# Kernel optimization log

Hardware: AMD Instinct MI355X
Metric: run time of the kernel (lower is better)

Reference implementation:

```python
import jax, jax.numpy as jnp
import numpy as np

NEG_INF_SCALE = -1e9  # matches mask * -1000000000.0 in the original


def setup_inputs() -> dict:
    key = jax.random.key(0)
    k1, k2, k3, k4 = jax.random.split(key, 4)
    B, H, S, D = 2, 16, 2048, 64
    return {
        "query": jax.random.normal(k1, (B, H, S, D), dtype=jnp.float32),
        "key": jax.random.normal(k2, (B, H, S, D), dtype=jnp.float32),
        "value": jax.random.normal(k3, (B, H, S, D), dtype=jnp.float32),
        "mask": jax.random.randint(k4, (B, 1, 1, S), 0, 2, dtype=jnp.int32),
    }


def reference(query, key, value, mask):
    head_dimension = query.shape[-1]
    scale = 1.0 / jnp.sqrt(jnp.float32(head_dimension))
    # (b h q d),(b h k d) -> (b h q k)
    logits = jnp.einsum("bhqd,bhkd->bhqk", query, key) * scale
    logits = logits + mask.astype(logits.dtype) * NEG_INF_SCALE
    attention_weights = jax.nn.softmax(logits, axis=-1)
    # (b h q k),(b h k d) -> (b h q d)
    output = jnp.einsum("bhqk,bhkd->bhqd", attention_weights, value)
    return output, attention_weights
```

## Files before the change

### kernel.cpp

```cpp
#include <hip/hip_runtime.h>

#define SEQ   2048
#define DIM   64
#define NB    2
#define NH    16
#define NHEAD (NB * NH)
#define BQ    128
#define BK    64
#define NKT   (SEQ / BK)
#define NQT   (SEQ / BQ)
#define QSCALE 0.18033688011112042f

typedef float  f32x4  __attribute__((ext_vector_type(4)));
typedef short  bf16x8 __attribute__((ext_vector_type(8)));
typedef unsigned short u16;
typedef u16    u16x4  __attribute__((ext_vector_type(4)));
typedef u16    u16x8  __attribute__((ext_vector_type(8)));
typedef unsigned int u32x4 __attribute__((ext_vector_type(4)));

__device__ __forceinline__ short f2bf(float x) {
    unsigned u = __float_as_uint(x);
    return (short)((u + 0x7FFFu + ((u >> 16) & 1u)) >> 16);
}

__device__ __forceinline__ unsigned cvtpk(float lo, float hi) {
    unsigned r;
    asm("v_cvt_pk_bf16_f32 %0, %1, %2" : "=v"(r) : "v"(lo), "v"(hi));
    return r;
}

__device__ __forceinline__ void gll16(const void* g, void* l) {
    __builtin_amdgcn_global_load_lds(
        (const __attribute__((address_space(1))) unsigned int*)g,
        (__attribute__((address_space(3))) unsigned int*)l, 16, 0, 0);
}

__global__ __launch_bounds__(256)
void conv_k_kernel(const float* __restrict__ K, u16* __restrict__ Kp)
{
    const int idx  = (int)blockIdx.x * 256 + (int)threadIdx.x;
    const int lane = idx & 63;
    const int s    = (idx >> 6) & 7;
    const int kt   = (idx >> 9) & 31;
    const int h    = idx >> 14;
    const int mrow = lane & 15;
    const int kg4  = (lane >> 4) << 2;
    const int row  = (s >> 1) * 16 + mrow;
    const int cb   = (s & 1) * 32 + kg4;

    const float* src = K + ((size_t)h * SEQ + (size_t)kt * 64 + row) * DIM + cb;
    const float4 a = *reinterpret_cast<const float4*>(src);
    const float4 b = *reinterpret_cast<const float4*>(src + 16);
    u16x8 o;
    o[0] = (u16)f2bf(a.x); o[1] = (u16)f2bf(a.y); o[2] = (u16)f2bf(a.z); o[3] = (u16)f2bf(a.w);
    o[4] = (u16)f2bf(b.x); o[5] = (u16)f2bf(b.y); o[6] = (u16)f2bf(b.z); o[7] = (u16)f2bf(b.w);
    *reinterpret_cast<u16x8*>(Kp + (size_t)idx * 8) = o;
}

__global__ __launch_bounds__(256)
void conv_v_kernel(const float* __restrict__ V, u16* __restrict__ Vp)
{
    const int idx  = (int)blockIdx.x * 256 + (int)threadIdx.x;
    const int lane = idx & 63;
    const int s    = (idx >> 6) & 7;
    const int kt   = (idx >> 9) & 31;
    const int h    = idx >> 14;
    const int mrow = lane & 15;
    const int kg4  = (lane >> 4) << 2;
    const int rd   = (s >> 1) * 16 + mrow;
    const int cb   = (s & 1) * 32 + kg4;

    const float* vb = V + ((size_t)h * SEQ + (size_t)kt * 64) * DIM;
    u16x8 o;
    #pragma unroll
    for (int j = 0; j < 4; ++j) {
        o[j]     = (u16)f2bf(vb[(size_t)(cb + j) * DIM + rd]);
        o[4 + j] = (u16)f2bf(vb[(size_t)(cb + 16 + j) * DIM + rd]);
    }
    *reinterpret_cast<u16x8*>(Vp + (size_t)idx * 8) = o;
}

__global__ __launch_bounds__(512, 4)
void sdpa_main_kernel(const float* __restrict__ Qp, const u16* __restrict__ Kp,
                      const u16* __restrict__ Vp, const int* __restrict__ Mp,
                      float* __restrict__ Op, float* __restrict__ Pg_)
{
    __shared__ u16   Ks[3][4096];
    __shared__ u16   Vs[3][4096];
    __shared__ float Fb[SEQ];
    __shared__ u16   Pst[8][16][68];

    const int tid  = (int)threadIdx.x;
    const int lane = tid & 63;
    const int w    = tid >> 6;
    const int mrow = lane & 15;
    const int kg4  = (lane >> 4) << 2;

    const int bid  = (int)blockIdx.x;
    const int xcd  = bid & 7;
    const int slot = bid >> 3;
    const int bh   = xcd * 4 + (slot >> 4);
    const int qt   = slot & 15;

    const size_t headoff = (size_t)bh * SEQ * DIM;
    const float* Qg = Qp + headoff + (size_t)qt * BQ * DIM;
    const u16*   Kh = Kp + (size_t)bh * NKT * 4096;
    const u16*   Vh = Vp + (size_t)bh * NKT * 4096;
    const int*   Mg = Mp + (size_t)(bh / NH) * SEQ;
    float*       Og = Op + headoff + (size_t)qt * BQ * DIM;
    float*       Pg = Pg_ + ((size_t)bh * SEQ + (size_t)qt * BQ) * SEQ;

    {
        const int4 m0 = *reinterpret_cast<const int4*>(Mg + tid * 4);
        float4 f0;
        f0.x = m0.x ? -1.0e9f : 0.0f; f0.y = m0.y ? -1.0e9f : 0.0f;
        f0.z = m0.z ? -1.0e9f : 0.0f; f0.w = m0.w ? -1.0e9f : 0.0f;
        *reinterpret_cast<float4*>(&Fb[tid * 4]) = f0;
    }

    bf16x8 qf0, qf1;
    {
        const float* qrow = Qg + (size_t)(w * 16 + mrow) * DIM;
        const float4 a = *reinterpret_cast<const float4*>(qrow + kg4);
        const float4 b = *reinterpret_cast<const float4*>(qrow + 16 + kg4);
        const float4 c = *reinterpret_cast<const float4*>(qrow + 32 + kg4);
        const float4 d = *reinterpret_cast<const float4*>(qrow + 48 + kg4);
        qf0[0] = f2bf(a.x * QSCALE); qf0[1] = f2bf(a.y * QSCALE);
        qf0[2] = f2bf(a.z * QSCALE); qf0[3] = f2bf(a.w * QSCALE);
        qf0[4] = f2bf(b.x * QSCALE); qf0[5] = f2bf(b.y * QSCALE);
        qf0[6] = f2bf(b.z * QSCALE); qf0[7] = f2bf(b.w * QSCALE);
        qf1[0] = f2bf(c.x * QSCALE); qf1[1] = f2bf(c.y * QSCALE);
        qf1[2] = f2bf(c.z * QSCALE); qf1[3] = f2bf(c.w * QSCALE);
        qf1[4] = f2bf(d.x * QSCALE); qf1[5] = f2bf(d.y * QSCALE);
        qf1[6] = f2bf(d.z * QSCALE); qf1[7] = f2bf(d.w * QSCALE);
    }
    __syncthreads();

    const int so  = tid * 8;
    const int lo8 = lane * 8;

    gll16(Kh + so, &Ks[0][so]);
    gll16(Kh + 4096 + so, &Ks[1][so]);

    float lsum = 0.f;
    int bcur = 0, bpre = 2;

    for (int kt = 0; kt < NKT; ++kt) {
        asm volatile("s_waitcnt vmcnt(1)" ::: "memory");
        __builtin_amdgcn_s_barrier();
        gll16(Kh + (size_t)((kt + 2) & (NKT - 1)) * 4096 + so, &Ks[bpre][so]);
        __builtin_amdgcn_sched_barrier(0);

        const u16* kp = &Ks[bcur][lo8];
        const int k0 = kt * BK;
        #pragma unroll
        for (int t = 0; t < 4; ++t) {
            const bf16x8 kf0 = *reinterpret_cast<const bf16x8*>(kp + (2 * t) * 512);
            const bf16x8 kf1 = *reinterpret_cast<const bf16x8*>(kp + (2 * t + 1) * 512);
            f32x4 a = {0.f, 0.f, 0.f, 0.f};
            a = __builtin_amdgcn_mfma_f32_16x16x32_bf16(kf0, qf0, a, 0, 0, 0);
            a = __builtin_amdgcn_mfma_f32_16x16x32_bf16(kf1, qf1, a, 0, 0, 0);
            const float4 b = *reinterpret_cast<const float4*>(&Fb[k0 + t * 16 + kg4]);
            lsum += __builtin_amdgcn_exp2f(a[0] + b.x);
            lsum += __builtin_amdgcn_exp2f(a[1] + b.y);
            lsum += __builtin_amdgcn_exp2f(a[2] + b.z);
            lsum += __builtin_amdgcn_exp2f(a[3] + b.w);
        }

        bcur = (bcur == 2) ? 0 : bcur + 1;
        bpre = (bpre == 2) ? 0 : bpre + 1;
    }

    asm volatile("s_waitcnt vmcnt(0)" ::: "memory");

    lsum += __shfl_xor(lsum, 16);
    lsum += __shfl_xor(lsum, 32);
    const float rinv = 1.0f / lsum;

    __builtin_amdgcn_s_barrier();

    f32x4 oacc[4];
    #pragma unroll
    for (int n = 0; n < 4; ++n) {
        oacc[n][0] = 0.f; oacc[n][1] = 0.f; oacc[n][2] = 0.f; oacc[n][3] = 0.f;
    }

    gll16(Kh + so, &Ks[0][so]);
    gll16(Vh + so, &Vs[0][so]);
    gll16(Kh + 4096 + so, &Ks[1][so]);
    gll16(Vh + 4096 + so, &Vs[1][so]);
    asm volatile("s_waitcnt vmcnt(2)" ::: "memory");
    __builtin_amdgcn_s_barrier();
    bcur = 0; bpre = 2;

    float* PgW = Pg + (size_t)(w * 16) * SEQ;

    for (int kt = 0; kt < NKT; ++kt) {
        if (kt == 1) { asm volatile("s_waitcnt vmcnt(6)" ::: "memory"); }
        else         { asm volatile("s_waitcnt vmcnt(10)" ::: "memory"); }
        __builtin_amdgcn_s_barrier();
        {
            const size_t nt = (size_t)((kt + 2) & (NKT - 1)) * 4096;
            gll16(Kh + nt + so, &Ks[bpre][so]);
            gll16(Vh + nt + so, &Vs[bpre][so]);
        }
        __builtin_amdgcn_sched_barrier(0);

        const u16* kp = &Ks[bcur][lo8];
        const u16* vp = &Vs[bcur][lo8];
        const int k0 = kt * BK;
        bf16x8 pf0, pf1;

        #pragma unroll
        for (int half = 0; half < 2; ++half) {
            f32x4 p[2];
            #pragma unroll
            for (int i = 0; i < 2; ++i) {
                const int t = half * 2 + i;
                const bf16x8 kf0 = *reinterpret_cast<const bf16x8*>(kp + (2 * t) * 512);
                const bf16x8 kf1 = *reinterpret_cast<const bf16x8*>(kp + (2 * t + 1) * 512);
                f32x4 a = {0.f, 0.f, 0.f, 0.f};
                a = __builtin_amdgcn_mfma_f32_16x16x32_bf16(kf0, qf0, a, 0, 0, 0);
                a = __builtin_amdgcn_mfma_f32_16x16x32_bf16(kf1, qf1, a, 0, 0, 0);
                const float4 b = *reinterpret_cast<const float4*>(&Fb[k0 + t * 16 + kg4]);
                p[i][0] = __builtin_amdgcn_exp2f(a[0] + b.x) * rinv;
                p[i][1] = __builtin_amdgcn_exp2f(a[1] + b.y) * rinv;
                p[i][2] = __builtin_amdgcn_exp2f(a[2] + b.z) * rinv;
                p[i][3] = __builtin_amdgcn_exp2f(a[3] + b.w) * rinv;
            }
            const u32x4 packed = { cvtpk(p[0][0], p[0][1]), cvtpk(p[0][2], p[0][3]),
                                   cvtpk(p[1][0], p[1][1]), cvtpk(p[1][2], p[1][3]) };
            if (half == 0) pf0 = __builtin_bit_cast(bf16x8, packed);
            else           pf1 = __builtin_bit_cast(bf16x8, packed);
        }

        {
            const u16x4* f0 = reinterpret_cast<const u16x4*>(&pf0);
            const u16x4* f1 = reinterpret_cast<const u16x4*>(&pf1);
            *reinterpret_cast<u16x4*>(&Pst[w][mrow][kg4])      = f0[0];
            *reinterpret_cast<u16x4*>(&Pst[w][mrow][16 + kg4]) = f0[1];
            *reinterpret_cast<u16x4*>(&Pst[w][mrow][32 + kg4]) = f1[0];
            *reinterpret_cast<u16x4*>(&Pst[w][mrow][48 + kg4]) = f1[1];
        }

        #pragma unroll
        for (int n = 0; n < 4; ++n) {
            const bf16x8 vf0 = *reinterpret_cast<const bf16x8*>(vp + (2 * n) * 512);
            const bf16x8 vf1 = *reinterpret_cast<const bf16x8*>(vp + (2 * n + 1) * 512);
            oacc[n] = __builtin_amdgcn_mfma_f32_16x16x32_bf16(pf0, vf0, oacc[n], 0, 0, 0);
            oacc[n] = __builtin_amdgcn_mfma_f32_16x16x32_bf16(pf1, vf1, oacc[n], 0, 0, 0);
        }

        #pragma unroll
        for (int j = 0; j < 4; ++j) {
            const u16x4 r = *reinterpret_cast<const u16x4*>(
                &Pst[w][j * 4 + (lane >> 4)][(lane & 15) * 4]);
            float4 f;
            f.x = __uint_as_float((unsigned)r[0] << 16);
            f.y = __uint_as_float((unsigned)r[1] << 16);
            f.z = __uint_as_float((unsigned)r[2] << 16);
            f.w = __uint_as_float((unsigned)r[3] << 16);
            *reinterpret_cast<float4*>(
                PgW + (size_t)(j * 4 + (lane >> 4)) * SEQ + k0 + 4 * (lane & 15)) = f;
        }

        bcur = (bcur == 2) ? 0 : bcur + 1;
        bpre = (bpre == 2) ? 0 : bpre + 1;
    }

    #pragma unroll
    for (int n = 0; n < 4; ++n) {
        #pragma unroll
        for (int r = 0; r < 4; ++r)
            Og[(size_t)(w * 16 + kg4 + r) * DIM + n * 16 + mrow] = oacc[n][r];
    }
}

extern "C" void kernel_launch(void* const* d_in, const int* in_sizes, int n_in,
                              void* d_out, int out_size, void* d_ws, size_t ws_size,
                              hipStream_t stream) {
    const float* Q = (const float*)d_in[0];
    const float* K = (const float*)d_in[1];
    const float* V = (const float*)d_in[2];
    const int*   M = (const int*)d_in[3];
    float* O = (float*)d_out;
    float* P = O + (size_t)NB * NH * SEQ * DIM;

    u16* Kp = (u16*)d_ws;
    u16* Vp = Kp + (size_t)NHEAD * SEQ * DIM;

    const int conv_blocks = NHEAD * NKT * 8 * 64 / 256;
    conv_k_kernel<<<dim3(conv_blocks), dim3(256), 0, stream>>>(K, Kp);
    conv_v_kernel<<<dim3(conv_blocks), dim3(256), 0, stream>>>(V, Vp);

    sdpa_main_kernel<<<dim3(NHEAD * NQT), dim3(512, 1, 1), 0, stream>>>(Q, Kp, Vp, M, O, P);
}
```

Measured before the change: 187.8 us.

## Double query tile to 256 rows with 1024-thread blocks sharing K/V tiles

Query tile grows from 128 to 256 rows. Each block now runs 16 waves at 1024 threads, so every K/V tile held in LDS serves twice as many query rows. Loading is split so waves 0-7 fetch K and waves 8-15 fetch V, and the vmcnt waits are adjusted to match. This halves LDS/global K/V traffic per query, but the grid shrinks to 256 blocks with one block per CU, which risks lower occupancy and less latency hiding.

```diff
diff --git a/kernel.cpp b/kernel.cpp
--- a/kernel.cpp
+++ b/kernel.cpp
@@ -5,7 +5,7 @@
 #define NB    2
 #define NH    16
 #define NHEAD (NB * NH)
-#define BQ    128
+#define BQ    256
 #define BK    64
 #define NKT   (SEQ / BK)
 #define NQT   (SEQ / BQ)
@@ -80,7 +80,7 @@
     *reinterpret_cast<u16x8*>(Vp + (size_t)idx * 8) = o;
 }
 
-__global__ __launch_bounds__(512, 4)
+__global__ __launch_bounds__(1024, 1)
 void sdpa_main_kernel(const float* __restrict__ Qp, const u16* __restrict__ Kp,
                       const u16* __restrict__ Vp, const int* __restrict__ Mp,
                       float* __restrict__ Op, float* __restrict__ Pg_)
@@ -88,7 +88,7 @@
     __shared__ u16   Ks[3][4096];
     __shared__ u16   Vs[3][4096];
     __shared__ float Fb[SEQ];
-    __shared__ u16   Pst[8][16][68];
+    __shared__ u16   Pst[16][16][68];
 
     const int tid  = (int)threadIdx.x;
     const int lane = tid & 63;
@@ -99,8 +99,8 @@
     const int bid  = (int)blockIdx.x;
     const int xcd  = bid & 7;
     const int slot = bid >> 3;
-    const int bh   = xcd * 4 + (slot >> 4);
-    const int qt   = slot & 15;
+    const int bh   = xcd * 4 + (slot >> 3);
+    const int qt   = slot & 7;
 
     const size_t headoff = (size_t)bh * SEQ * DIM;
     const float* Qg = Qp + headoff + (size_t)qt * BQ * DIM;
@@ -111,11 +111,11 @@
     float*       Pg = Pg_ + ((size_t)bh * SEQ + (size_t)qt * BQ) * SEQ;
 
     {
-        const int4 m0 = *reinterpret_cast<const int4*>(Mg + tid * 4);
-        float4 f0;
-        f0.x = m0.x ? -1.0e9f : 0.0f; f0.y = m0.y ? -1.0e9f : 0.0f;
-        f0.z = m0.z ? -1.0e9f : 0.0f; f0.w = m0.w ? -1.0e9f : 0.0f;
-        *reinterpret_cast<float4*>(&Fb[tid * 4]) = f0;
+        const int2 m0 = *reinterpret_cast<const int2*>(Mg + tid * 2);
+        float2 f0;
+        f0.x = m0.x ? -1.0e9f : 0.0f;
+        f0.y = m0.y ? -1.0e9f : 0.0f;
+        *reinterpret_cast<float2*>(&Fb[tid * 2]) = f0;
     }
 
     bf16x8 qf0, qf1;
@@ -136,11 +136,13 @@
     }
     __syncthreads();
 
-    const int so  = tid * 8;
+    const int so8 = (tid & 511) * 8;
     const int lo8 = lane * 8;
 
-    gll16(Kh + so, &Ks[0][so]);
-    gll16(Kh + 4096 + so, &Ks[1][so]);
+    if (w < 8) {
+        gll16(Kh + so8, &Ks[0][so8]);
+        gll16(Kh + 4096 + so8, &Ks[1][so8]);
+    }
 
     float lsum = 0.f;
     int bcur = 0, bpre = 2;
@@ -148,7 +150,8 @@
     for (int kt = 0; kt < NKT; ++kt) {
         asm volatile("s_waitcnt vmcnt(1)" ::: "memory");
         __builtin_amdgcn_s_barrier();
-        gll16(Kh + (size_t)((kt + 2) & (NKT - 1)) * 4096 + so, &Ks[bpre][so]);
+        if (w < 8)
+            gll16(Kh + (size_t)((kt + 2) & (NKT - 1)) * 4096 + so8, &Ks[bpre][so8]);
         __builtin_amdgcn_sched_barrier(0);
 
         const u16* kp = &Ks[bcur][lo8];
@@ -185,24 +188,27 @@
         oacc[n][0] = 0.f; oacc[n][1] = 0.f; oacc[n][2] = 0.f; oacc[n][3] = 0.f;
     }
 
-    gll16(Kh + so, &Ks[0][so]);
-    gll16(Vh + so, &Vs[0][so]);
-    gll16(Kh + 4096 + so, &Ks[1][so]);
-    gll16(Vh + 4096 + so, &Vs[1][so]);
-    asm volatile("s_waitcnt vmcnt(2)" ::: "memory");
+    if (w < 8) {
+        gll16(Kh + so8, &Ks[0][so8]);
+        gll16(Kh + 4096 + so8, &Ks[1][so8]);
+    } else {
+        gll16(Vh + so8, &Vs[0][so8]);
+        gll16(Vh + 4096 + so8, &Vs[1][so8]);
+    }
+    asm volatile("s_waitcnt vmcnt(1)" ::: "memory");
     __builtin_amdgcn_s_barrier();
     bcur = 0; bpre = 2;
 
     float* PgW = Pg + (size_t)(w * 16) * SEQ;
 
     for (int kt = 0; kt < NKT; ++kt) {
-        if (kt == 1) { asm volatile("s_waitcnt vmcnt(6)" ::: "memory"); }
-        else         { asm volatile("s_waitcnt vmcnt(10)" ::: "memory"); }
+        if (kt == 1) { asm volatile("s_waitcnt vmcnt(5)" ::: "memory"); }
+        else         { asm volatile("s_waitcnt vmcnt(9)" ::: "memory"); }
         __builtin_amdgcn_s_barrier();
         {
             const size_t nt = (size_t)((kt + 2) & (NKT - 1)) * 4096;
-            gll16(Kh + nt + so, &Ks[bpre][so]);
-            gll16(Vh + nt + so, &Vs[bpre][so]);
+            if (w < 8) gll16(Kh + nt + so8, &Ks[bpre][so8]);
+            else       gll16(Vh + nt + so8, &Vs[bpre][so8]);
         }
         __builtin_amdgcn_sched_barrier(0);
 
@@ -293,5 +299,5 @@
     conv_k_kernel<<<dim3(conv_blocks), dim3(256), 0, stream>>>(K, Kp);
     conv_v_kernel<<<dim3(conv_blocks), dim3(256), 0, stream>>>(V, Vp);
 
-    sdpa_main_kernel<<<dim3(NHEAD * NQT), dim3(512, 1, 1), 0, stream>>>(Q, Kp, Vp, M, O, P);
-}
+    sdpa_main_kernel<<<dim3(NHEAD * NQT), dim3(1024, 1, 1), 0, stream>>>(Q, Kp, Vp, M, O, P);
+}
```

Result: faster. 182.3 us (-2.9%).
